# Kernel optimization log

Hardware: AMD Instinct MI355X
Metric: run time of the kernel (lower is better)

## Reference

```python
import jax, jax.numpy as jnp
import numpy as np

B, T, C, H = 4, 2048, 1024, 16
D = C // H  # head dim = 64


def setup_inputs() -> dict:
    key = jax.random.key(0)
    ks = jax.random.split(key, 8)
    s = 1.0 / np.sqrt(C)
    return {
        "x": jax.random.normal(ks[0], (B, T, C), jnp.float32),
        "mask": jax.random.randint(ks[1], (B, T), 0, 2, jnp.int32),
        "Wq": jax.random.normal(ks[2], (C, C), jnp.float32) * s,
        "bq": jnp.zeros((C,), jnp.float32),
        "Wk": jax.random.normal(ks[3], (C, C), jnp.float32) * s,
        "bk": jnp.zeros((C,), jnp.float32),
        "Wv": jax.random.normal(ks[4], (C, C), jnp.float32) * s,
        "bv": jnp.zeros((C,), jnp.float32),
    }


def reference(x, mask, Wq, bq, Wk, bk, Wv, bv):
    # QKV projections (nn.Linear: x @ W.T + b); W stored here as [out,in] -> use W.T
    q = x @ Wq.T + bq
    k = x @ Wk.T + bk
    v = x @ Wv.T + bv
    # split heads: [B,T,C] -> [B,H,T,D]
    q = q.reshape(B, T, H, D).transpose(0, 2, 1, 3)
    k = k.reshape(B, T, H, D).transpose(0, 2, 1, 3)
    v = v.reshape(B, T, H, D).transpose(0, 2, 1, 3)
    # scaled dot-product attention scores [B,H,T,T]
    attn = jnp.einsum("bhqd,bhkd->bhqk", q, k) / jnp.sqrt(jnp.float32(D))
    # additive mask over key positions: attn - inf*(1-mask), expressed stably
    big_neg = jnp.float32(-1e30)
    attn = jnp.where(mask[:, None, None, :] > 0, attn, big_neg)
    attn = jax.nn.softmax(attn, axis=-1)
    # dropout p=0 -> identity
    y = jnp.einsum("bhqk,bhkd->bhqd", attn, v)
    # merge heads: [B,H,T,D] -> [B,T,C]
    return y.transpose(0, 2, 1, 3).reshape(B, T, C)
```

## Files before the change

### kernel.cpp

```cpp
#include <hip/hip_runtime.h>
#include <stdint.h>

#define BB 4
#define TT 2048
#define CC 1024
#define HH 16
#define DD 64
#define MM (BB * TT)

typedef unsigned short u16;
typedef unsigned int   u32;
typedef __attribute__((ext_vector_type(8))) short short8;
typedef _Float16 half8  __attribute__((ext_vector_type(8)));
typedef __fp16   fp16x2 __attribute__((ext_vector_type(2)));
typedef __attribute__((ext_vector_type(4))) float f32x4;
typedef __attribute__((ext_vector_type(4))) unsigned short u16x4;
typedef __attribute__((ext_vector_type(4))) unsigned int u32x4;

#if __has_builtin(__builtin_amdgcn_exp2f)
#define EXP2(x) __builtin_amdgcn_exp2f(x)
#else
#define EXP2(x) __expf(0.69314718055994531f * (x))
#endif

__device__ inline u16 f2bf(float f) {
    union { float f; unsigned u; } v; v.f = f;
    unsigned r = 0x7fffu + ((v.u >> 16) & 1u);
    return (u16)((v.u + r) >> 16);
}
__device__ inline u16 f2h(float f) {
    union { _Float16 h; u16 u; } c; c.h = (_Float16)f; return c.u;
}
__device__ inline u32 pkh(float a, float b) {
    union { fp16x2 h; u32 u; } c;
    c.h = __builtin_amdgcn_cvt_pkrtz(a, b);
    return c.u;
}

#define NX (MM * CC / 4)
#define NW (CC * CC / 4)
__global__ void cvt_all(const float* __restrict__ x,  const float* __restrict__ Wq,
                        const float* __restrict__ Wk, const float* __restrict__ Wv,
                        u16* __restrict__ xb, u16* __restrict__ Wb) {
    int i = blockIdx.x * blockDim.x + threadIdx.x;
    const float* src; u16* dst; int j;
    if (i < NX)               { src = x;  dst = xb;                       j = i; }
    else if (i < NX + NW)     { src = Wq; dst = Wb;                       j = i - NX; }
    else if (i < NX + 2 * NW) { src = Wk; dst = Wb + (size_t)CC * CC;     j = i - NX - NW; }
    else if (i < NX + 3 * NW) { src = Wv; dst = Wb + (size_t)2 * CC * CC; j = i - NX - 2 * NW; }
    else return;
    float4 v = ((const float4*)src)[j];
    u16x4 o;
    o.x = f2bf(v.x); o.y = f2bf(v.y); o.z = f2bf(v.z); o.w = f2bf(v.w);
    ((u16x4*)dst)[j] = o;
}

__global__ void qkv_gemm(const u16* __restrict__ xb, const u16* __restrict__ Wb,
                         const float* __restrict__ bq, const float* __restrict__ bk,
                         const float* __restrict__ bv,
                         u16* __restrict__ Qh, u16* __restrict__ Kh, u16* __restrict__ Vt)
{
    const int z = blockIdx.z;
    const u16* W = Wb + (size_t)z * CC * CC;
    const float* bias = (z == 0) ? bq : ((z == 1) ? bk : bv);
    const float scale = (z == 0) ? 0.18033688011112042f : 1.0f;

    __shared__ __align__(16) u16 As[128][32];
    __shared__ __align__(16) u16 Bs[128][32];

    const int tid = threadIdx.x;
    const int l  = tid & 63, w = tid >> 6;
    const int wm = w >> 1,  wn = w & 1;
    const int lr = l & 15,  lq = l >> 4;
    const int m0 = blockIdx.y * 128, n0 = blockIdx.x * 128;

    f32x4 acc[4][4] = {};

    const u16* aLDS = (z == 2) ? &As[0][0] : &Bs[0][0];
    const u16* bLDS = (z == 2) ? &Bs[0][0] : &As[0][0];

    for (int kt = 0; kt < CC; kt += 32) {
        __syncthreads();
        #pragma unroll
        for (int r = 0; r < 2; ++r) {
            int c   = (r * 4 + w) * 64 + l;
            int row = c >> 2, kc = c & 3;
            const u16* ga = xb + (size_t)(m0 + row) * CC + kt + kc * 8;
            __builtin_amdgcn_global_load_lds(
                (const __attribute__((address_space(1))) void*)ga,
                (__attribute__((address_space(3))) void*)(&As[0][0] + (size_t)c * 8), 16, 0, 0);
            const u16* gb = W + (size_t)(n0 + row) * CC + kt + kc * 8;
            __builtin_amdgcn_global_load_lds(
                (const __attribute__((address_space(1))) void*)gb,
                (__attribute__((address_space(3))) void*)(&Bs[0][0] + (size_t)c * 8), 16, 0, 0);
        }
        __syncthreads();

        short8 af[4], bfr[4];
        #pragma unroll
        for (int mi = 0; mi < 4; ++mi)
            af[mi] = *(const short8*)(aLDS + (size_t)(wm * 64 + mi * 16 + lr) * 32 + lq * 8);
        #pragma unroll
        for (int ni = 0; ni < 4; ++ni)
            bfr[ni] = *(const short8*)(bLDS + (size_t)(wn * 64 + ni * 16 + lr) * 32 + lq * 8);
        #pragma unroll
        for (int mi = 0; mi < 4; ++mi)
            #pragma unroll
            for (int ni = 0; ni < 4; ++ni)
                acc[mi][ni] = __builtin_amdgcn_mfma_f32_16x16x32_bf16(
                    af[mi], bfr[ni], acc[mi][ni], 0, 0, 0);
    }

    if (z == 2) {
        #pragma unroll
        for (int ni = 0; ni < 4; ++ni) {
            int n = n0 + wn * 64 + ni * 16 + lr;
            float bvv = bias[n];
            int h = n >> 6, d = n & 63;
            #pragma unroll
            for (int mi = 0; mi < 4; ++mi) {
                int mbase = m0 + wm * 64 + mi * 16 + lq * 4;
                int b = mbase >> 11, t0 = mbase & (TT - 1);
                u16x4 pkv;
                #pragma unroll
                for (int r = 0; r < 4; ++r)
                    pkv[r] = f2h(acc[mi][ni][r] + bvv);
                *(u16x4*)&Vt[((size_t)(b * HH + h) * DD + d) * TT + t0] = pkv;
            }
        }
    } else {
        u16* out = (z == 0) ? Qh : Kh;
        #pragma unroll
        for (int mi = 0; mi < 4; ++mi) {
            int nb = n0 + wm * 64 + mi * 16 + lq * 4;
            float4 b4 = *(const float4*)&bias[nb];
            int h = nb >> 6, d0 = nb & 63;
            #pragma unroll
            for (int ni = 0; ni < 4; ++ni) {
                int m = m0 + wn * 64 + ni * 16 + lr;
                int b = m >> 11, t = m & (TT - 1);
                u16x4 pkv;
                pkv.x = f2h((acc[mi][ni][0] + b4.x) * scale);
                pkv.y = f2h((acc[mi][ni][1] + b4.y) * scale);
                pkv.z = f2h((acc[mi][ni][2] + b4.z) * scale);
                pkv.w = f2h((acc[mi][ni][3] + b4.w) * scale);
                *(u16x4*)&out[((size_t)(b * HH + h) * TT + t) * DD + d0] = pkv;
            }
        }
    }
}

__global__ __launch_bounds__(256, 2)
void attn_kernel(const u16* __restrict__ Qh, const u16* __restrict__ Kh,
                 const u16* __restrict__ Vt, const int* __restrict__ mask,
                 float* __restrict__ out)
{
    const int qt = blockIdx.x;
    const int h  = blockIdx.y;
    const int b  = blockIdx.z;
    const int tid = threadIdx.x;
    const int l  = tid & 63, w = tid >> 6;
    const int lr = l & 15,  lq = l >> 4;

    __shared__ __align__(16) u16 Ks[2][32][72];
    __shared__ __align__(16) u16 Vs[2][80][40];

    const size_t base = (size_t)(b * HH + h) * TT * DD;
    const int q0 = qt * 256 + w * 64;

    half8 qf[4][2];
    #pragma unroll
    for (int qg = 0; qg < 4; ++qg)
        #pragma unroll
        for (int c = 0; c < 2; ++c)
            qf[qg][c] = *(const half8*)(Qh + base + (size_t)(q0 + qg * 16 + lr) * DD
                                        + c * 32 + lq * 8);

    const int kk = tid >> 3, dc = tid & 7;
    u16* k_dst0 = &Ks[0][kk][dc * 8];
    const u16* k_base = Kh + base + (size_t)kk * DD + dc * 8;
    const int vd = tid >> 2, vck = tid & 3;
    const int s0c = ((2 * vck) & 3) * 8 + (vck >> 1) * 4;
    const int s1c = ((2 * vck + 1) & 3) * 8 + (vck >> 1) * 4;
    u16* v_dst0a = &Vs[0][vd][s0c];
    u16* v_dst0b = &Vs[0][vd][s1c];
    const u16* v_base = Vt + base + (size_t)vd * TT + vck * 8;
    const int* mbase_p = mask + b * TT + 4 * lq;

    for (int i = tid; i < 16 * 40; i += 256) {
        (&Vs[0][64][0])[i] = 0x3C00;
        (&Vs[1][64][0])[i] = 0x3C00;
    }

    {
        half8 k0 = *(const half8*)k_base;
        half8 v0 = *(const half8*)v_base;
        *(half8*)k_dst0 = k0;
        u16x4 va = { (u16)((u32x4&)v0)[0], (u16)(((u32x4&)v0)[0] >> 16),
                     (u16)((u32x4&)v0)[1], (u16)(((u32x4&)v0)[1] >> 16) };
        u16x4 vb = { (u16)((u32x4&)v0)[2], (u16)(((u32x4&)v0)[2] >> 16),
                     (u16)((u32x4&)v0)[3], (u16)(((u32x4&)v0)[3] >> 16) };
        *(u16x4*)v_dst0a = va;
        *(u16x4*)v_dst0b = vb;
    }

    f32x4 o[4][5] = {};

    const int NT = TT / 32;
    __syncthreads();

    for (int kt = 0; kt < NT; ++kt) {
        const int p = kt & 1;
        int ktn = (kt + 1 < NT) ? kt + 1 : NT - 1;
        half8 kreg = *(const half8*)(k_base + (size_t)ktn * 32 * DD);
        half8 vreg = *(const half8*)(v_base + ktn * 32);
        int4 ma = *(const int4*)(mbase_p + kt * 32);
        int4 mb = *(const int4*)(mbase_p + kt * 32 + 16);

        half8 kf[2][2];
        #pragma unroll
        for (int kg = 0; kg < 2; ++kg)
            #pragma unroll
            for (int c = 0; c < 2; ++c)
                kf[kg][c] = *(const half8*)&Ks[p][kg * 16 + lr][c * 32 + lq * 8];

        f32x4 s[2][4];
        #pragma unroll
        for (int kg = 0; kg < 2; ++kg)
            #pragma unroll
            for (int qg = 0; qg < 4; ++qg) {
                f32x4 zz = {};
                zz = __builtin_amdgcn_mfma_f32_16x16x32_f16(kf[kg][0], qf[qg][0], zz, 0, 0, 0);
                zz = __builtin_amdgcn_mfma_f32_16x16x32_f16(kf[kg][1], qf[qg][1], zz, 0, 0, 0);
                s[kg][qg] = zz;
            }

        float f00 = (float)ma.x, f01 = (float)ma.y, f02 = (float)ma.z, f03 = (float)ma.w;
        float f10 = (float)mb.x, f11 = (float)mb.y, f12 = (float)mb.z, f13 = (float)mb.w;
        half8 pf[4];
        #pragma unroll
        for (int qg = 0; qg < 4; ++qg) {
            u32x4 pk;
            pk[0] = pkh(EXP2(s[0][qg][0]) * f00, EXP2(s[0][qg][1]) * f01);
            pk[1] = pkh(EXP2(s[0][qg][2]) * f02, EXP2(s[0][qg][3]) * f03);
            pk[2] = pkh(EXP2(s[1][qg][0]) * f10, EXP2(s[1][qg][1]) * f11);
            pk[3] = pkh(EXP2(s[1][qg][2]) * f12, EXP2(s[1][qg][3]) * f13);
            pf[qg] = (half8&)pk;
        }

        #pragma unroll
        for (int dg = 0; dg < 5; ++dg) {
            half8 vf = *(const half8*)&Vs[p][dg * 16 + lr][lq * 8];
            #pragma unroll
            for (int qg = 0; qg < 4; ++qg)
                o[qg][dg] = __builtin_amdgcn_mfma_f32_16x16x32_f16(pf[qg], vf, o[qg][dg], 0, 0, 0);
        }

        *(half8*)(k_dst0 + (p ^ 1) * (32 * 72)) = kreg;
        u16x4 va = { (u16)((u32x4&)vreg)[0], (u16)(((u32x4&)vreg)[0] >> 16),
                     (u16)((u32x4&)vreg)[1], (u16)(((u32x4&)vreg)[1] >> 16) };
        u16x4 vb = { (u16)((u32x4&)vreg)[2], (u16)(((u32x4&)vreg)[2] >> 16),
                     (u16)((u32x4&)vreg)[3], (u16)(((u32x4&)vreg)[3] >> 16) };
        *(u16x4*)(v_dst0a + (p ^ 1) * (80 * 40)) = va;
        *(u16x4*)(v_dst0b + (p ^ 1) * (80 * 40)) = vb;
        __syncthreads();
    }

    #pragma unroll
    for (int qg = 0; qg < 4; ++qg)
        #pragma unroll
        for (int r = 0; r < 4; ++r) {
            float inv = 1.f / o[qg][4][r];
            int t = q0 + qg * 16 + lq * 4 + r;
            float* op = out + (size_t)(b * TT + t) * CC + h * DD;
            #pragma unroll
            for (int dg = 0; dg < 4; ++dg)
                op[dg * 16 + lr] = o[qg][dg][r] * inv;
        }
}

extern "C" void kernel_launch(void* const* d_in, const int* in_sizes, int n_in,
                              void* d_out, int out_size, void* d_ws, size_t ws_size,
                              hipStream_t stream) {
    const float* x    = (const float*)d_in[0];
    const int*   mask = (const int*)d_in[1];
    const float* Wq   = (const float*)d_in[2];
    const float* bq   = (const float*)d_in[3];
    const float* Wk   = (const float*)d_in[4];
    const float* bk   = (const float*)d_in[5];
    const float* Wv   = (const float*)d_in[6];
    const float* bv   = (const float*)d_in[7];
    float* out = (float*)d_out;

    u16* xb = (u16*)d_ws;
    u16* Wb = xb + (size_t)MM * CC;
    u16* Qh = Wb + (size_t)3 * CC * CC;
    u16* Kh = Qh + (size_t)MM * CC;
    u16* Vt = Kh + (size_t)MM * CC;

    {
        int total = NX + 3 * NW;
        cvt_all<<<(total + 255) / 256, 256, 0, stream>>>(x, Wq, Wk, Wv, xb, Wb);
    }

    qkv_gemm<<<dim3(CC / 128, MM / 128, 3), 256, 0, stream>>>(xb, Wb, bq, bk, bv, Qh, Kh, Vt);

    attn_kernel<<<dim3(TT / 256, HH, BB), 256, 0, stream>>>(Qh, Kh, Vt, mask, out);
}
```

Baseline: 252.6 us.

## Stream K/V tiles into LDS via direct global-to-LDS loads with XOR swizzle

The attention kernel now loads K and V tiles with global_load_lds straight into unpadded, XOR-swizzled LDS buffers instead of staging them through registers and writing them back. To make the direct copy line up with the MFMA operand layout, the V-projection epilogue writes Vt with its time index pre-permuted inside each 32-element group. The row-sum column of ones is no longer stored in LDS; it is supplied as a register constant in a separate MFMA. This is meant to cut register pressure, VALU repacking and LDS bank conflicts, but it ties the Vt layout to the swizzle and relies on the async loads being complete at the barrier.

```diff
diff --git a/kernel.cpp b/kernel.cpp
--- a/kernel.cpp
+++ b/kernel.cpp
@@ -35,6 +35,10 @@
     union { fp16x2 h; u32 u; } c;
     c.h = __builtin_amdgcn_cvt_pkrtz(a, b);
     return c.u;
+}
+__device__ inline void load_lds16(const u16* g, u16* l) {
+    __builtin_amdgcn_global_load_lds((const __attribute__((address_space(1))) void*)g,
+                                     (__attribute__((address_space(3))) void*)l, 16, 0, 0);
 }
 
 #define NX (MM * CC / 4)
@@ -86,13 +90,9 @@
             int c   = (r * 4 + w) * 64 + l;
             int row = c >> 2, kc = c & 3;
             const u16* ga = xb + (size_t)(m0 + row) * CC + kt + kc * 8;
-            __builtin_amdgcn_global_load_lds(
-                (const __attribute__((address_space(1))) void*)ga,
-                (__attribute__((address_space(3))) void*)(&As[0][0] + (size_t)c * 8), 16, 0, 0);
+            load_lds16(ga, &As[0][0] + (size_t)c * 8);
             const u16* gb = W + (size_t)(n0 + row) * CC + kt + kc * 8;
-            __builtin_amdgcn_global_load_lds(
-                (const __attribute__((address_space(1))) void*)gb,
-                (__attribute__((address_space(3))) void*)(&Bs[0][0] + (size_t)c * 8), 16, 0, 0);
+            load_lds16(gb, &Bs[0][0] + (size_t)c * 8);
         }
         __syncthreads();
 
@@ -121,11 +121,13 @@
             for (int mi = 0; mi < 4; ++mi) {
                 int mbase = m0 + wm * 64 + mi * 16 + lq * 4;
                 int b = mbase >> 11, t0 = mbase & (TT - 1);
+                int tg = t0 & ~31;
+                int s0 = (((t0 >> 2) & 3) << 3) + (((t0 >> 4) & 1) << 2);
                 u16x4 pkv;
                 #pragma unroll
                 for (int r = 0; r < 4; ++r)
                     pkv[r] = f2h(acc[mi][ni][r] + bvv);
-                *(u16x4*)&Vt[((size_t)(b * HH + h) * DD + d) * TT + t0] = pkv;
+                *(u16x4*)&Vt[((size_t)(b * HH + h) * DD + d) * TT + tg + s0] = pkv;
             }
         }
     } else {
@@ -162,8 +164,8 @@
     const int l  = tid & 63, w = tid >> 6;
     const int lr = l & 15,  lq = l >> 4;
 
-    __shared__ __align__(16) u16 Ks[2][32][72];
-    __shared__ __align__(16) u16 Vs[2][80][40];
+    __shared__ __align__(16) u16 KsL[2][32 * 64];
+    __shared__ __align__(16) u16 VsL[2][64 * 32];
 
     const size_t base = (size_t)(b * HH + h) * TT * DD;
     const int q0 = qt * 256 + w * 64;
@@ -176,53 +178,46 @@
             qf[qg][c] = *(const half8*)(Qh + base + (size_t)(q0 + qg * 16 + lr) * DD
                                         + c * 32 + lq * 8);
 
-    const int kk = tid >> 3, dc = tid & 7;
-    u16* k_dst0 = &Ks[0][kk][dc * 8];
-    const u16* k_base = Kh + base + (size_t)kk * DD + dc * 8;
-    const int vd = tid >> 2, vck = tid & 3;
-    const int s0c = ((2 * vck) & 3) * 8 + (vck >> 1) * 4;
-    const int s1c = ((2 * vck + 1) & 3) * 8 + (vck >> 1) * 4;
-    u16* v_dst0a = &Vs[0][vd][s0c];
-    u16* v_dst0b = &Vs[0][vd][s1c];
-    const u16* v_base = Vt + base + (size_t)vd * TT + vck * 8;
+    const int kkey = tid >> 3, kqx = tid & 7;
+    const int kq = kqx ^ (kkey & 7);
+    const u16* kgp = Kh + base + (size_t)kkey * DD + kq * 8;
+    u16* kl0 = &KsL[0][0] + tid * 8;
+    const int vdd = tid >> 2, vqx = tid & 3;
+    const int vq = vqx ^ ((vdd >> 1) & 3);
+    const u16* vgp = Vt + base + (size_t)vdd * TT + vq * 8;
+    u16* vl0 = &VsL[0][0] + tid * 8;
+
     const int* mbase_p = mask + b * TT + 4 * lq;
 
-    for (int i = tid; i < 16 * 40; i += 256) {
-        (&Vs[0][64][0])[i] = 0x3C00;
-        (&Vs[1][64][0])[i] = 0x3C00;
-    }
-
-    {
-        half8 k0 = *(const half8*)k_base;
-        half8 v0 = *(const half8*)v_base;
-        *(half8*)k_dst0 = k0;
-        u16x4 va = { (u16)((u32x4&)v0)[0], (u16)(((u32x4&)v0)[0] >> 16),
-                     (u16)((u32x4&)v0)[1], (u16)(((u32x4&)v0)[1] >> 16) };
-        u16x4 vb = { (u16)((u32x4&)v0)[2], (u16)(((u32x4&)v0)[2] >> 16),
-                     (u16)((u32x4&)v0)[3], (u16)(((u32x4&)v0)[3] >> 16) };
-        *(u16x4*)v_dst0a = va;
-        *(u16x4*)v_dst0b = vb;
-    }
+    u32x4 onesbits = { 0x3C003C00u, 0x3C003C00u, 0x3C003C00u, 0x3C003C00u };
+    half8 ones = (half8&)onesbits;
 
     f32x4 o[4][5] = {};
 
     const int NT = TT / 32;
+
+    load_lds16(kgp, kl0);
+    load_lds16(vgp, vl0);
     __syncthreads();
 
     for (int kt = 0; kt < NT; ++kt) {
         const int p = kt & 1;
-        int ktn = (kt + 1 < NT) ? kt + 1 : NT - 1;
-        half8 kreg = *(const half8*)(k_base + (size_t)ktn * 32 * DD);
-        half8 vreg = *(const half8*)(v_base + ktn * 32);
+        if (kt + 1 < NT) {
+            load_lds16(kgp + (size_t)(kt + 1) * 32 * DD, kl0 + (p ^ 1) * (32 * 64));
+            load_lds16(vgp + (size_t)(kt + 1) * 32,      vl0 + (p ^ 1) * (64 * 32));
+        }
         int4 ma = *(const int4*)(mbase_p + kt * 32);
         int4 mb = *(const int4*)(mbase_p + kt * 32 + 16);
 
         half8 kf[2][2];
         #pragma unroll
-        for (int kg = 0; kg < 2; ++kg)
+        for (int kg = 0; kg < 2; ++kg) {
+            int key = kg * 16 + lr;
             #pragma unroll
             for (int c = 0; c < 2; ++c)
-                kf[kg][c] = *(const half8*)&Ks[p][kg * 16 + lr][c * 32 + lq * 8];
+                kf[kg][c] = *(const half8*)&KsL[p][key * 64
+                                + (((c * 4 + lq) ^ (key & 7)) * 8)];
+        }
 
         f32x4 s[2][4];
         #pragma unroll
@@ -249,20 +244,17 @@
         }
 
         #pragma unroll
-        for (int dg = 0; dg < 5; ++dg) {
-            half8 vf = *(const half8*)&Vs[p][dg * 16 + lr][lq * 8];
+        for (int dg = 0; dg < 4; ++dg) {
+            int d = dg * 16 + lr;
+            half8 vf = *(const half8*)&VsL[p][d * 32 + ((lq ^ ((d >> 1) & 3)) * 8)];
             #pragma unroll
             for (int qg = 0; qg < 4; ++qg)
                 o[qg][dg] = __builtin_amdgcn_mfma_f32_16x16x32_f16(pf[qg], vf, o[qg][dg], 0, 0, 0);
         }
-
-        *(half8*)(k_dst0 + (p ^ 1) * (32 * 72)) = kreg;
-        u16x4 va = { (u16)((u32x4&)vreg)[0], (u16)(((u32x4&)vreg)[0] >> 16),
-                     (u16)((u32x4&)vreg)[1], (u16)(((u32x4&)vreg)[1] >> 16) };
-        u16x4 vb = { (u16)((u32x4&)vreg)[2], (u16)(((u32x4&)vreg)[2] >> 16),
-                     (u16)((u32x4&)vreg)[3], (u16)(((u32x4&)vreg)[3] >> 16) };
-        *(u16x4*)(v_dst0a + (p ^ 1) * (80 * 40)) = va;
-        *(u16x4*)(v_dst0b + (p ^ 1) * (80 * 40)) = vb;
+        #pragma unroll
+        for (int qg = 0; qg < 4; ++qg)
+            o[qg][4] = __builtin_amdgcn_mfma_f32_16x16x32_f16(pf[qg], ones, o[qg][4], 0, 0, 0);
+
         __syncthreads();
     }
 
```

Result: no change. 256.2 us (+1.4%).
